# Kernel optimization log

Measured on AMD Instinct MI355X. Metric: run time of the kernel, lower is better.

## Reference

```python
import jax, jax.numpy as jnp
import numpy as np

NUM_FEATURES = 1024
NUM_TRAINING = 32768
NUM_EPOCHS = 2
STEP_SIZE = 0.01


def setup_inputs() -> dict:
    key = jax.random.key(0)
    k1, k2, k3 = jax.random.split(key, 3)
    data = jax.random.normal(k1, (NUM_TRAINING, NUM_FEATURES), dtype=jnp.float32)
    label = jax.random.uniform(k2, (NUM_TRAINING,), dtype=jnp.float32)
    theta = jax.random.normal(k3, (NUM_FEATURES,), dtype=jnp.float32)
    return {"data": data, "label": label, "theta": theta}


def reference(data, label, theta):
    data_2d = data.reshape(NUM_TRAINING, NUM_FEATURES)

    def sample_step(theta, xs):
        x, y = xs  # x: [F], y: scalar
        prob = jax.nn.sigmoid(jnp.dot(theta, x))
        theta = theta - STEP_SIZE * (prob - y) * x
        return theta, None

    def epoch_step(theta, _):
        theta, _ = jax.lax.scan(sample_step, theta, (data_2d, label))
        return theta, None

    theta, _ = jax.lax.scan(epoch_step, theta, None, length=NUM_EPOCHS)
    return theta
```

## Files before the change

kernel.cpp:

```cpp
#include <hip/hip_runtime.h>
#include <hip/hip_cooperative_groups.h>

namespace cg = cooperative_groups;

#define F 1024
#define NTRAIN 32768
#define EPOCHS 2
#define STEP 0.01f
#define BB 512
#define NBLK (NTRAIN / BB)
#define PHASES (EPOCHS * NBLK)
#define COOP_WGS 32

__device__ __forceinline__ float rdlane(float v, int lane) {
    return __uint_as_float(__builtin_amdgcn_readlane(__float_as_uint(v), (unsigned)lane));
}

__global__ __launch_bounds__(256) void gram_kernel(const float* __restrict__ X,
                                                   float* __restrict__ G)
{
    const int wg  = blockIdx.x;
    const int b   = wg / 36;
    int tij = wg % 36;
    int ti = 0;
    while (tij >= 8 - ti) { tij -= 8 - ti; ++ti; }
    const int tj = ti + tij;

    __shared__ __align__(16) float At[16][68];
    __shared__ __align__(16) float Bt[16][68];

    const int t  = threadIdx.x;
    const int tx = t & 15, ty = t >> 4;
    const int sr = t >> 2, sc = (t & 3) * 4;

    const float* Xa = X + (size_t)(b * BB + ti * 64) * F;
    const float* Xb = X + (size_t)(b * BB + tj * 64) * F;
    float* Gb = G + (size_t)b * BB * BB;

    float acc[4][4];
#pragma unroll
    for (int p = 0; p < 4; ++p)
#pragma unroll
        for (int q = 0; q < 4; ++q) acc[p][q] = 0.f;

    for (int kc = 0; kc < F; kc += 16) {
        float4 va = *(const float4*)(Xa + (size_t)sr * F + kc + sc);
        float4 vb = *(const float4*)(Xb + (size_t)sr * F + kc + sc);
        __syncthreads();
        At[sc + 0][sr] = va.x; At[sc + 1][sr] = va.y; At[sc + 2][sr] = va.z; At[sc + 3][sr] = va.w;
        Bt[sc + 0][sr] = vb.x; Bt[sc + 1][sr] = vb.y; Bt[sc + 2][sr] = vb.z; Bt[sc + 3][sr] = vb.w;
        __syncthreads();
#pragma unroll
        for (int k = 0; k < 16; ++k) {
            float4 a4 = *(const float4*)&At[k][ty * 4];
            float4 b4 = *(const float4*)&Bt[k][tx * 4];
            acc[0][0] = fmaf(a4.x, b4.x, acc[0][0]);
            acc[0][1] = fmaf(a4.x, b4.y, acc[0][1]);
            acc[0][2] = fmaf(a4.x, b4.z, acc[0][2]);
            acc[0][3] = fmaf(a4.x, b4.w, acc[0][3]);
            acc[1][0] = fmaf(a4.y, b4.x, acc[1][0]);
            acc[1][1] = fmaf(a4.y, b4.y, acc[1][1]);
            acc[1][2] = fmaf(a4.y, b4.z, acc[1][2]);
            acc[1][3] = fmaf(a4.y, b4.w, acc[1][3]);
            acc[2][0] = fmaf(a4.z, b4.x, acc[2][0]);
            acc[2][1] = fmaf(a4.z, b4.y, acc[2][1]);
            acc[2][2] = fmaf(a4.z, b4.z, acc[2][2]);
            acc[2][3] = fmaf(a4.z, b4.w, acc[2][3]);
            acc[3][0] = fmaf(a4.w, b4.x, acc[3][0]);
            acc[3][1] = fmaf(a4.w, b4.y, acc[3][1]);
            acc[3][2] = fmaf(a4.w, b4.z, acc[3][2]);
            acc[3][3] = fmaf(a4.w, b4.w, acc[3][3]);
        }
    }

#pragma unroll
    for (int p = 0; p < 4; ++p) {
        int i = ti * 64 + ty * 4 + p;
        float4 v = make_float4(acc[p][0], acc[p][1], acc[p][2], acc[p][3]);
        *(float4*)(Gb + (size_t)i * BB + tj * 64 + tx * 4) = v;
    }
    if (ti != tj) {
#pragma unroll
        for (int p = 0; p < 4; ++p)
#pragma unroll
            for (int q = 0; q < 4; ++q)
                Gb[(size_t)(tj * 64 + tx * 4 + q) * BB + ti * 64 + ty * 4 + p] = acc[p][q];
    }
}

__global__ __launch_bounds__(256) void sgd_coop(
    const float* __restrict__ X, const float* __restrict__ label,
    const float* __restrict__ theta0, float* __restrict__ out,
    const float* __restrict__ G, float* __restrict__ theta,
    float* __restrict__ sbuf, float* __restrict__ wbuf)
{
    cg::grid_group grid = cg::this_grid();
    const int tid = threadIdx.x;
    const int wg  = blockIdx.x;

    if (wg < 4) theta[wg * 256 + tid] = theta0[wg * 256 + tid];
    grid.sync();

    auto sgemv = [&](int blk) {
        const int wv = (wg << 2) | (tid >> 6);
        const int L  = tid & 63;
        const float4* th4 = (const float4*)theta;
        float4 t4[4];
#pragma unroll
        for (int m = 0; m < 4; ++m) t4[m] = th4[L + 64 * m];
        for (int rr = 0; rr < 4; ++rr) {
            const int r = wv * 4 + rr;
            const float4* xr = (const float4*)(X + (size_t)(blk * BB + r) * F);
            float acc = 0.f;
#pragma unroll
            for (int m = 0; m < 4; ++m) {
                float4 x4 = xr[L + 64 * m];
                acc = fmaf(x4.x, t4[m].x, acc);
                acc = fmaf(x4.y, t4[m].y, acc);
                acc = fmaf(x4.z, t4[m].z, acc);
                acc = fmaf(x4.w, t4[m].w, acc);
            }
#pragma unroll
            for (int off = 32; off > 0; off >>= 1)
                acc += __shfl_xor(acc, off, 64);
            if (L == 0) sbuf[r] = acc;
        }
    };

    sgemv(0);
    grid.sync();

    for (int p = 0; p < PHASES; ++p) {
        const int blk = p & (NBLK - 1);

        if (wg == 0 && tid < 64) {
            const int L = tid;
            const float* Gb = G + (size_t)blk * BB * BB;
            const float4* s4 = (const float4*)sbuf;
            float4 z04 = s4[L * 2], z14 = s4[L * 2 + 1];
            float zac[8] = {z04.x, z04.y, z04.z, z04.w, z14.x, z14.y, z14.z, z14.w};
            const float4* y4 = (const float4*)(label + blk * BB);
            float4 ya = y4[L * 2], yb = y4[L * 2 + 1];
            float yv[8] = {ya.x, ya.y, ya.z, ya.w, yb.x, yb.y, yb.z, yb.w};

            float4 gb0[8], gb1[8];
#pragma unroll
            for (int u = 0; u < 8; ++u) {
                const float4* gr = (const float4*)(Gb + (size_t)u * BB) + L * 2;
                gb0[u] = gr[0]; gb1[u] = gr[1];
            }

            for (int i8 = 0; i8 < 64; ++i8) {
                float wout[8];
#pragma unroll
                for (int u = 0; u < 8; ++u) {
                    float zi = rdlane(zac[u], i8);
                    float yi = rdlane(yv[u], i8);
                    float E    = __builtin_amdgcn_exp2f(zi * -1.44269504088896f);
                    float prob = __builtin_amdgcn_rcpf(1.0f + E);
                    float wv   = STEP * (yi - prob);
                    wout[u] = wv;
                    float4 g0 = gb0[u], g1 = gb1[u];
                    zac[0] = fmaf(wv, g0.x, zac[0]);
                    zac[1] = fmaf(wv, g0.y, zac[1]);
                    zac[2] = fmaf(wv, g0.z, zac[2]);
                    zac[3] = fmaf(wv, g0.w, zac[3]);
                    zac[4] = fmaf(wv, g1.x, zac[4]);
                    zac[5] = fmaf(wv, g1.y, zac[5]);
                    zac[6] = fmaf(wv, g1.z, zac[6]);
                    zac[7] = fmaf(wv, g1.w, zac[7]);
                    if (i8 < 63) {
                        const float4* gr =
                            (const float4*)(Gb + (size_t)((i8 + 1) * 8 + u) * BB) + L * 2;
                        gb0[u] = gr[0]; gb1[u] = gr[1];
                    }
                }
                if (L == i8) {
                    float4* wp = (float4*)(wbuf + i8 * 8);
                    wp[0] = make_float4(wout[0], wout[1], wout[2], wout[3]);
                    wp[1] = make_float4(wout[4], wout[5], wout[6], wout[7]);
                }
            }
        }
        grid.sync();

        if (wg < 16) {
            __shared__ float red[4][64];
            const int j  = wg * 64 + (tid & 63);
            const int rg = tid >> 6;
            const float* Xb = X + (size_t)blk * BB * F;
            float acc = 0.f;
            for (int ii = 0; ii < 128; ++ii) {
                const int i = rg * 128 + ii;
                acc = fmaf(wbuf[i], Xb[(size_t)i * F + j], acc);
            }
            red[rg][tid & 63] = acc;
            __syncthreads();
            if (tid < 64) {
                float v = theta[j] + red[0][tid] + red[1][tid] + red[2][tid] + red[3][tid];
                theta[j] = v;
                if (p == PHASES - 1) out[j] = v;
            }
        }
        grid.sync();

        if (p + 1 < PHASES) sgemv((p + 1) & (NBLK - 1));
        grid.sync();
    }
}

__global__ __launch_bounds__(64, 1) void sgd_seq_kernel(
    const float* __restrict__ data, const float* __restrict__ label,
    const float* __restrict__ theta_in, float* __restrict__ theta_out)
{
    const int lane = threadIdx.x;
    const float4* data4  = (const float4*)data;
    const float4* th4_in = (const float4*)theta_in;
    float4 th[4];
#pragma unroll
    for (int j = 0; j < 4; ++j) th[j] = th4_in[j * 64 + lane];
    float4 xv[4], xn[4];
#pragma unroll
    for (int j = 0; j < 4; ++j) xv[j] = data4[j * 64 + lane];
    float y = label[0];
    const int total = EPOCHS * NTRAIN;
    for (int it = 0; it < total; ++it) {
        int nn = it + 1;
        int nidx = (nn >= total) ? 0 : (nn & (NTRAIN - 1));
        const float4* xp = data4 + (size_t)nidx * (F / 4);
#pragma unroll
        for (int j = 0; j < 4; ++j) xn[j] = xp[j * 64 + lane];
        float ynext = label[nidx];
        float p0 = xv[0].x * th[0].x; p0 = fmaf(xv[0].y, th[0].y, p0);
        p0 = fmaf(xv[0].z, th[0].z, p0); p0 = fmaf(xv[0].w, th[0].w, p0);
        float p1 = xv[1].x * th[1].x; p1 = fmaf(xv[1].y, th[1].y, p1);
        p1 = fmaf(xv[1].z, th[1].z, p1); p1 = fmaf(xv[1].w, th[1].w, p1);
        float p2 = xv[2].x * th[2].x; p2 = fmaf(xv[2].y, th[2].y, p2);
        p2 = fmaf(xv[2].z, th[2].z, p2); p2 = fmaf(xv[2].w, th[2].w, p2);
        float p3 = xv[3].x * th[3].x; p3 = fmaf(xv[3].y, th[3].y, p3);
        p3 = fmaf(xv[3].z, th[3].z, p3); p3 = fmaf(xv[3].w, th[3].w, p3);
        float p = (p0 + p1) + (p2 + p3);
#pragma unroll
        for (int off = 32; off > 0; off >>= 1) p += __shfl_xor(p, off, 64);
        float e = __builtin_amdgcn_exp2f(-p * 1.44269504088896f);
        float prob = __builtin_amdgcn_rcpf(1.0f + e);
        float c = STEP * (prob - y);
#pragma unroll
        for (int j = 0; j < 4; ++j) {
            th[j].x = fmaf(-c, xv[j].x, th[j].x);
            th[j].y = fmaf(-c, xv[j].y, th[j].y);
            th[j].z = fmaf(-c, xv[j].z, th[j].z);
            th[j].w = fmaf(-c, xv[j].w, th[j].w);
        }
#pragma unroll
        for (int j = 0; j < 4; ++j) xv[j] = xn[j];
        y = ynext;
    }
    float4* out4 = (float4*)theta_out;
#pragma unroll
    for (int j = 0; j < 4; ++j) out4[j * 64 + lane] = th[j];
}

extern "C" void kernel_launch(void* const* d_in, const int* in_sizes, int n_in,
                              void* d_out, int out_size, void* d_ws, size_t ws_size,
                              hipStream_t stream) {
    (void)in_sizes; (void)n_in; (void)out_size;
    const float* X      = (const float*)d_in[0];
    const float* label  = (const float*)d_in[1];
    const float* theta0 = (const float*)d_in[2];
    float* out = (float*)d_out;

    const size_t gsz  = (size_t)NBLK * BB * BB;
    const size_t need = (gsz + F + BB + BB) * sizeof(float);

    if (ws_size < need) {
        sgd_seq_kernel<<<1, 64, 0, stream>>>(X, label, theta0, out);
        return;
    }

    float* G     = (float*)d_ws;
    float* theta = G + gsz;
    float* sbuf  = theta + F;
    float* wbuf  = sbuf + BB;

    gram_kernel<<<NBLK * 36, 256, 0, stream>>>(X, G);

    void* args[] = {(void*)&X, (void*)&label, (void*)&theta0, (void*)&out,
                    (void*)&G, (void*)&theta, (void*)&sbuf, (void*)&wbuf};
    hipLaunchCooperativeKernel((void*)sgd_coop, dim3(COOP_WGS), dim3(256),
                               args, 0, stream);
}
```

Baseline: 6.892 ms.

## Precompute next-block logits via cross-Gram and overlap with sequential solve

Adds cross-block Gram tiles C (next block rows times current block rows) to the gram kernel. The new cooperative kernel has the other workgroups compute the next block's logits against the old theta while workgroup 0 runs the sequential 512-sample recurrence. The next block's starting logits are then fixed up with C·w instead of a full 512x1024 sgemv after each theta update. This takes the sgemv off the critical path between phases. It also folds the -log2e and step-size constants into the recurrence to shorten the serial dependency chain. The cost is twice the workspace, extra Gram work for C, and a larger gram launch.

```diff
diff --git a/kernel.cpp b/kernel.cpp
--- a/kernel.cpp
+++ b/kernel.cpp
@@ -12,19 +12,32 @@
 #define PHASES (EPOCHS * NBLK)
 #define COOP_WGS 32
 
+#define NL2E 1.4426950408889634f
+#define C1K  0.014426950408889634f
+#define NLN2 0.69314718055994531f
+
 __device__ __forceinline__ float rdlane(float v, int lane) {
     return __uint_as_float(__builtin_amdgcn_readlane(__float_as_uint(v), (unsigned)lane));
 }
 
 __global__ __launch_bounds__(256) void gram_kernel(const float* __restrict__ X,
-                                                   float* __restrict__ G)
+                                                   float* __restrict__ G,
+                                                   float* __restrict__ C,
+                                                   int tiles_per_b)
 {
     const int wg  = blockIdx.x;
-    const int b   = wg / 36;
-    int tij = wg % 36;
-    int ti = 0;
-    while (tij >= 8 - ti) { tij -= 8 - ti; ++ti; }
-    const int tj = ti + tij;
+    const int b   = wg / tiles_per_b;
+    int rem = wg % tiles_per_b;
+
+    int ti, tj;
+    bool isC = (rem >= 36);
+    if (!isC) {
+        int tij = rem; ti = 0;
+        while (tij >= 8 - ti) { tij -= 8 - ti; ++ti; }
+        tj = ti + tij;
+    } else {
+        rem -= 36; ti = rem >> 3; tj = rem & 7;
+    }
 
     __shared__ __align__(16) float At[16][68];
     __shared__ __align__(16) float Bt[16][68];
@@ -33,9 +46,10 @@
     const int tx = t & 15, ty = t >> 4;
     const int sr = t >> 2, sc = (t & 3) * 4;
 
-    const float* Xa = X + (size_t)(b * BB + ti * 64) * F;
+    const int rowBlk = isC ? ((b + 1) & (NBLK - 1)) : b;
+    const float* Xa = X + (size_t)(rowBlk * BB + ti * 64) * F;
     const float* Xb = X + (size_t)(b * BB + tj * 64) * F;
-    float* Gb = G + (size_t)b * BB * BB;
+    float* Ob = (isC ? C : G) + (size_t)b * BB * BB;
 
     float acc[4][4];
 #pragma unroll
@@ -77,14 +91,180 @@
     for (int p = 0; p < 4; ++p) {
         int i = ti * 64 + ty * 4 + p;
         float4 v = make_float4(acc[p][0], acc[p][1], acc[p][2], acc[p][3]);
-        *(float4*)(Gb + (size_t)i * BB + tj * 64 + tx * 4) = v;
-    }
-    if (ti != tj) {
+        *(float4*)(Ob + (size_t)i * BB + tj * 64 + tx * 4) = v;
+    }
+    if (!isC && ti != tj) {
 #pragma unroll
         for (int p = 0; p < 4; ++p)
 #pragma unroll
             for (int q = 0; q < 4; ++q)
-                Gb[(size_t)(tj * 64 + tx * 4 + q) * BB + ti * 64 + ty * 4 + p] = acc[p][q];
+                Ob[(size_t)(tj * 64 + tx * 4 + q) * BB + ti * 64 + ty * 4 + p] = acc[p][q];
+    }
+}
+
+__global__ __launch_bounds__(256) void sgd_coop2(
+    const float* __restrict__ X, const float* __restrict__ label,
+    const float* __restrict__ theta0, float* __restrict__ out,
+    const float* __restrict__ G, const float* __restrict__ C,
+    float* __restrict__ theta, float* __restrict__ sbuf,
+    float* __restrict__ spre, float* __restrict__ wbuf)
+{
+    cg::grid_group grid = cg::this_grid();
+    const int tid = threadIdx.x;
+    const int wg  = blockIdx.x;
+
+    if (wg < 4) theta[wg * 256 + tid] = theta0[wg * 256 + tid];
+    grid.sync();
+
+    {
+        const int wv = (wg << 2) | (tid >> 6);
+        const int L  = tid & 63;
+        const float4* th4 = (const float4*)theta;
+        float4 t4[4];
+#pragma unroll
+        for (int m = 0; m < 4; ++m) t4[m] = th4[L + 64 * m];
+        for (int rr = 0; rr < 4; ++rr) {
+            const int r = wv * 4 + rr;
+            const float4* xr = (const float4*)(X + (size_t)r * F);
+            float acc = 0.f;
+#pragma unroll
+            for (int m = 0; m < 4; ++m) {
+                float4 x4 = xr[L + 64 * m];
+                acc = fmaf(x4.x, t4[m].x, acc);
+                acc = fmaf(x4.y, t4[m].y, acc);
+                acc = fmaf(x4.z, t4[m].z, acc);
+                acc = fmaf(x4.w, t4[m].w, acc);
+            }
+#pragma unroll
+            for (int off = 32; off > 0; off >>= 1)
+                acc += __shfl_xor(acc, off, 64);
+            if (L == 0) sbuf[r] = acc;
+        }
+    }
+    grid.sync();
+
+    for (int p = 0; p < PHASES; ++p) {
+        const int blk = p & (NBLK - 1);
+
+        if (wg == 0) {
+            if (tid < 64) {
+                const int L = tid;
+                const float* Gb = G + (size_t)blk * BB * BB;
+                const float4* s4 = (const float4*)sbuf;
+                float4 z04 = s4[L * 2], z14 = s4[L * 2 + 1];
+                float zac[8] = {-NL2E * z04.x, -NL2E * z04.y, -NL2E * z04.z, -NL2E * z04.w,
+                                -NL2E * z14.x, -NL2E * z14.y, -NL2E * z14.z, -NL2E * z14.w};
+                const float4* y4 = (const float4*)(label + blk * BB);
+                float4 ya = y4[L * 2], yb = y4[L * 2 + 1];
+                float c2[8] = {-C1K * ya.x, -C1K * ya.y, -C1K * ya.z, -C1K * ya.w,
+                               -C1K * yb.x, -C1K * yb.y, -C1K * yb.z, -C1K * yb.w};
+
+                float4 gb0[8], gb1[8];
+#pragma unroll
+                for (int u = 0; u < 8; ++u) {
+                    const float4* gr = (const float4*)(Gb + (size_t)u * BB) + L * 2;
+                    gb0[u] = gr[0]; gb1[u] = gr[1];
+                }
+
+                for (int i8 = 0; i8 < 64; ++i8) {
+                    float wout[8];
+#pragma unroll
+                    for (int u = 0; u < 8; ++u) {
+                        float zs = rdlane(zac[u], i8);
+                        float cc = rdlane(c2[u], i8);
+                        float E    = __builtin_amdgcn_exp2f(zs);
+                        float prob = __builtin_amdgcn_rcpf(1.0f + E);
+                        float wv2  = fmaf(C1K, prob, cc);
+                        wout[u] = wv2 * -NLN2;
+                        float ga[8] = {gb0[u].x, gb0[u].y, gb0[u].z, gb0[u].w,
+                                       gb1[u].x, gb1[u].y, gb1[u].z, gb1[u].w};
+#pragma unroll
+                        for (int jj = 0; jj < 8; ++jj) {
+                            int j = (u + 1 + jj) & 7;
+                            zac[j] = fmaf(wv2, ga[j], zac[j]);
+                        }
+                        if (i8 < 63) {
+                            const float4* gr =
+                                (const float4*)(Gb + (size_t)((i8 + 1) * 8 + u) * BB) + L * 2;
+                            gb0[u] = gr[0]; gb1[u] = gr[1];
+                        }
+                    }
+                    if (L == i8) {
+                        float4* wp = (float4*)(wbuf + i8 * 8);
+                        wp[0] = make_float4(wout[0], wout[1], wout[2], wout[3]);
+                        wp[1] = make_float4(wout[4], wout[5], wout[6], wout[7]);
+                    }
+                }
+            }
+        } else if (p + 1 < PHASES) {
+            const int w = (wg - 1) * 4 + (tid >> 6);
+            const int L = tid & 63;
+            const int nblk = (p + 1) & (NBLK - 1);
+            const float4* th4 = (const float4*)theta;
+            float4 t4[4];
+#pragma unroll
+            for (int m = 0; m < 4; ++m) t4[m] = th4[L + 64 * m];
+            for (int r = w; r < BB; r += 124) {
+                const float4* xr = (const float4*)(X + (size_t)(nblk * BB + r) * F);
+                float acc = 0.f;
+#pragma unroll
+                for (int m = 0; m < 4; ++m) {
+                    float4 x4 = xr[L + 64 * m];
+                    acc = fmaf(x4.x, t4[m].x, acc);
+                    acc = fmaf(x4.y, t4[m].y, acc);
+                    acc = fmaf(x4.z, t4[m].z, acc);
+                    acc = fmaf(x4.w, t4[m].w, acc);
+                }
+#pragma unroll
+                for (int off = 32; off > 0; off >>= 1)
+                    acc += __shfl_xor(acc, off, 64);
+                if (L == 0) spre[r] = acc;
+            }
+        }
+        grid.sync();
+
+        if (wg < 16) {
+            __shared__ float red[4][64];
+            const int j  = wg * 64 + (tid & 63);
+            const int rg = tid >> 6;
+            const float* Xb = X + (size_t)blk * BB * F;
+            float acc = 0.f;
+            for (int ii = 0; ii < 128; ++ii) {
+                const int i = rg * 128 + ii;
+                acc = fmaf(wbuf[i], Xb[(size_t)i * F + j], acc);
+            }
+            red[rg][tid & 63] = acc;
+            __syncthreads();
+            if (tid < 64) {
+                float v = theta[j] + red[0][tid] + red[1][tid] + red[2][tid] + red[3][tid];
+                theta[j] = v;
+                if (p == PHASES - 1) out[j] = v;
+            }
+        } else if (p + 1 < PHASES) {
+            const int w2 = (wg - 16) * 4 + (tid >> 6);
+            const int L  = tid & 63;
+            const float* Cb = C + (size_t)blk * BB * BB;
+            const float4* w4 = (const float4*)wbuf;
+            float4 wa = w4[L * 2], wb4 = w4[L * 2 + 1];
+            for (int rr = 0; rr < 8; ++rr) {
+                const int r = w2 * 8 + rr;
+                const float4* cr = (const float4*)(Cb + (size_t)r * BB) + L * 2;
+                float4 c0 = cr[0], c1r = cr[1];
+                float acc = c0.x * wa.x;
+                acc = fmaf(c0.y, wa.y, acc);
+                acc = fmaf(c0.z, wa.z, acc);
+                acc = fmaf(c0.w, wa.w, acc);
+                acc = fmaf(c1r.x, wb4.x, acc);
+                acc = fmaf(c1r.y, wb4.y, acc);
+                acc = fmaf(c1r.z, wb4.z, acc);
+                acc = fmaf(c1r.w, wb4.w, acc);
+#pragma unroll
+                for (int off = 32; off > 0; off >>= 1)
+                    acc += __shfl_xor(acc, off, 64);
+                if (L == 0) sbuf[r] = spre[r] + acc;
+            }
+        }
+        grid.sync();
     }
 }
 
@@ -132,7 +312,6 @@
 
     for (int p = 0; p < PHASES; ++p) {
         const int blk = p & (NBLK - 1);
-
         if (wg == 0 && tid < 64) {
             const int L = tid;
             const float* Gb = G + (size_t)blk * BB * BB;
@@ -142,21 +321,19 @@
             const float4* y4 = (const float4*)(label + blk * BB);
             float4 ya = y4[L * 2], yb = y4[L * 2 + 1];
             float yv[8] = {ya.x, ya.y, ya.z, ya.w, yb.x, yb.y, yb.z, yb.w};
-
             float4 gb0[8], gb1[8];
 #pragma unroll
             for (int u = 0; u < 8; ++u) {
                 const float4* gr = (const float4*)(Gb + (size_t)u * BB) + L * 2;
                 gb0[u] = gr[0]; gb1[u] = gr[1];
             }
-
             for (int i8 = 0; i8 < 64; ++i8) {
                 float wout[8];
 #pragma unroll
                 for (int u = 0; u < 8; ++u) {
                     float zi = rdlane(zac[u], i8);
                     float yi = rdlane(yv[u], i8);
-                    float E    = __builtin_amdgcn_exp2f(zi * -1.44269504088896f);
+                    float E    = __builtin_amdgcn_exp2f(zi * -NL2E);
                     float prob = __builtin_amdgcn_rcpf(1.0f + E);
                     float wv   = STEP * (yi - prob);
                     wout[u] = wv;
@@ -242,7 +419,7 @@
         float p = (p0 + p1) + (p2 + p3);
 #pragma unroll
         for (int off = 32; off > 0; off >>= 1) p += __shfl_xor(p, off, 64);
-        float e = __builtin_amdgcn_exp2f(-p * 1.44269504088896f);
+        float e = __builtin_amdgcn_exp2f(-p * NL2E);
         float prob = __builtin_amdgcn_rcpf(1.0f + e);
         float c = STEP * (prob - y);
 #pragma unroll
@@ -270,23 +447,37 @@
     const float* theta0 = (const float*)d_in[2];
     float* out = (float*)d_out;
 
-    const size_t gsz  = (size_t)NBLK * BB * BB;
-    const size_t need = (gsz + F + BB + BB) * sizeof(float);
-
-    if (ws_size < need) {
+    const size_t gsz   = (size_t)NBLK * BB * BB;
+    const size_t need2 = (2 * gsz + F + 3 * BB) * sizeof(float);
+    const size_t need1 = (gsz + F + 2 * BB) * sizeof(float);
+
+    if (ws_size >= need2) {
+        float* G     = (float*)d_ws;
+        float* C     = G + gsz;
+        float* theta = C + gsz;
+        float* sbuf  = theta + F;
+        float* spre  = sbuf + BB;
+        float* wbuf  = spre + BB;
+        int tiles = 100;
+        gram_kernel<<<NBLK * 100, 256, 0, stream>>>(X, G, C, tiles);
+        const float* Gc = G; const float* Cc = C;
+        void* args[] = {(void*)&X, (void*)&label, (void*)&theta0, (void*)&out,
+                        (void*)&Gc, (void*)&Cc, (void*)&theta, (void*)&sbuf,
+                        (void*)&spre, (void*)&wbuf};
+        hipLaunchCooperativeKernel((void*)sgd_coop2, dim3(COOP_WGS), dim3(256),
+                                   args, 0, stream);
+    } else if (ws_size >= need1) {
+        float* G     = (float*)d_ws;
+        float* theta = G + gsz;
+        float* sbuf  = theta + F;
+        float* wbuf  = sbuf + BB;
+        int tiles = 36;
+        gram_kernel<<<NBLK * 36, 256, 0, stream>>>(X, G, nullptr, tiles);
+        void* args[] = {(void*)&X, (void*)&label, (void*)&theta0, (void*)&out,
+                        (void*)&G, (void*)&theta, (void*)&sbuf, (void*)&wbuf};
+        hipLaunchCooperativeKernel((void*)sgd_coop, dim3(COOP_WGS), dim3(256),
+                                   args, 0, stream);
+    } else {
         sgd_seq_kernel<<<1, 64, 0, stream>>>(X, label, theta0, out);
-        return;
-    }
-
-    float* G     = (float*)d_ws;
-    float* theta = G + gsz;
-    float* sbuf  = theta + F;
-    float* wbuf  = sbuf + BB;
-
-    gram_kernel<<<NBLK * 36, 256, 0, stream>>>(X, G);
-
-    void* args[] = {(void*)&X, (void*)&label, (void*)&theta0, (void*)&out,
-                    (void*)&G, (void*)&theta, (void*)&sbuf, (void*)&wbuf};
-    hipLaunchCooperativeKernel((void*)sgd_coop, dim3(COOP_WGS), dim3(256),
-                               args, 0, stream);
-}
+    }
+}
```

New measurement: 6.713 ms. -2.6%, faster.
